# Optimization experiments

Hardware: AMD Instinct MI355X
Metric: run time of the kernel (lower is better)

## Reference

```python
import math
import jax, jax.numpy as jnp
import numpy as np

C = 1024
H = 8
EPS = 1e-5
SLOPE = 0.1


def _branch(x, W, gamma, beta, mean, var):
    # conv1x1 (no bias) -> BatchNorm1d (eval-mode stats) -> LeakyReLU(0.1)
    # x: [b, C, p], W: [C_out, C_in]
    y = jnp.einsum('oc,bcp->bop', W, x)
    scale = gamma / jnp.sqrt(var + EPS)          # [C]
    y = y * scale[:, None] + (beta - mean * scale)[:, None]
    return jnp.where(y > 0, y, SLOPE * y)


def setup_inputs() -> dict:
    key = jax.random.key(0)
    ks = jax.random.split(key, 20)
    b, pq, pk = 4, 2048, 2048
    d = {
        'Xq': jax.random.normal(ks[0], (b, C, pq), dtype=jnp.float32),
        'Xk': jax.random.normal(ks[1], (b, C, pk), dtype=jnp.float32),
        'Wq': jax.random.normal(ks[2], (C, C), dtype=jnp.float32) * (1.0 / math.sqrt(C)),
        'Wk': jax.random.normal(ks[3], (C, C), dtype=jnp.float32) * (1.0 / math.sqrt(C)),
        'Wv': jax.random.normal(ks[4], (C, C), dtype=jnp.float32) * (1.0 / math.sqrt(C)),
    }
    for i, tag in enumerate(['1', '2', '3']):
        d['gamma' + tag] = jnp.ones((C,), jnp.float32) + 0.1 * jax.random.normal(ks[5 + 4 * i], (C,), jnp.float32)
        d['beta' + tag] = 0.1 * jax.random.normal(ks[6 + 4 * i], (C,), jnp.float32)
        d['mean' + tag] = 0.1 * jax.random.normal(ks[7 + 4 * i], (C,), jnp.float32)
        d['var' + tag] = 0.5 + jax.random.uniform(ks[8 + 4 * i], (C,), jnp.float32)
    return d


def reference(Xq, Xk, Wq, Wk, Wv,
              gamma1, beta1, mean1, var1,
              gamma2, beta2, mean2, var2,
              gamma3, beta3, mean3, var3):
    Q = _branch(Xq, Wq, gamma1, beta1, mean1, var1)   # [b, C, pq]
    K = _branch(Xk, Wk, gamma2, beta2, mean2, var2)   # [b, C, pk]
    V = _branch(Xq, Wv, gamma3, beta3, mean3, var3)   # [b, C, pq]
    b, c, pk = K.shape
    pq = V.shape[-1]
    dh = c // H
    Qh = Q.reshape(b, H, dh, pq)
    Kh = K.reshape(b, H, dh, pk)
    Vh = V.reshape(b, H, dh, pq)
    # scores over channel dim: [b, h, pk, pq]
    Hmat = jnp.einsum('bhci,bhcj->bhij', Kh, Vh) / math.sqrt(c / H)
    Hmat = jax.nn.softmax(Hmat, axis=-1)
    out = jnp.einsum('bhij,bhcj->bhci', Hmat, Qh)     # [b, h, dh, pk]
    return out.reshape(b, c, pk)
```

## Files before the change

kernel.cpp:

```cpp
#include <hip/hip_runtime.h>

typedef __bf16 bf16_t;
typedef __bf16 bf16x8 __attribute__((ext_vector_type(8)));
typedef __bf16 bf16x4 __attribute__((ext_vector_type(4)));
typedef float  f32x4  __attribute__((ext_vector_type(4)));

#define WB_OFF  0LL
#define XQT_OFF 3145728LL
#define XKT_OFF 11534336LL
#define Q_OFF   19922944LL
#define KT_OFF  28311552LL
#define VT_OFF  36700160LL

__device__ __forceinline__ void gl_lds16(const bf16_t* g, bf16_t* l) {
  __builtin_amdgcn_global_load_lds((const __attribute__((address_space(1))) void*)(g),
                                   (__attribute__((address_space(3))) void*)(l), 16, 0, 0);
}

__device__ __forceinline__ bf16x4 cvt4(f32x4 v) {
  bf16x4 r;
  r[0] = (bf16_t)v[0]; r[1] = (bf16_t)v[1]; r[2] = (bf16_t)v[2]; r[3] = (bf16_t)v[3];
  return r;
}

__global__ __launch_bounds__(256) void k_wconv(
    const float* __restrict__ Wq, const float* __restrict__ Wk, const float* __restrict__ Wv,
    bf16_t* __restrict__ ws)
{
  const float* W = blockIdx.y == 0 ? Wq : (blockIdx.y == 1 ? Wk : Wv);
  bf16_t* dst = ws + WB_OFF + (long)blockIdx.y * 1048576;
  const long i = ((long)blockIdx.x * 256 + threadIdx.x) * 4;
  *(bf16x4*)&dst[i] = cvt4(*(const f32x4*)(W + i));
}

__global__ __launch_bounds__(256) void k_transpose(
    const float* __restrict__ Xq, const float* __restrict__ Xk, bf16_t* __restrict__ ws)
{
  __shared__ __align__(16) bf16_t t[64 * 72];
  const int z = blockIdx.z, b = z & 3, ts = z >> 2;
  const float* X = ts ? Xk : Xq;
  bf16_t* XT = ws + (ts ? XKT_OFF : XQT_OFF);
  const int p0 = blockIdx.x * 64, c0 = blockIdx.y * 64;
  const int tid = threadIdx.x;
  const int tx = tid & 15, ty = tid >> 4;
  const float* src = X + ((long)b * 1024 + c0) * 2048 + p0;
  #pragma unroll
  for (int hh = 0; hh < 4; ++hh) {
    int c = ty + hh * 16;
    f32x4 v = *(const f32x4*)(src + (long)c * 2048 + tx * 4);
    *(bf16x4*)&t[c * 72 + tx * 4] = cvt4(v);
  }
  __syncthreads();
  bf16_t* dst = XT + ((long)b * 2048 + p0) * 1024 + c0;
  #pragma unroll
  for (int hh = 0; hh < 2; ++hh) {
    int p = (tid >> 3) + hh * 32;
    int cc = tid & 7;
    bf16x8 v;
    #pragma unroll
    for (int j = 0; j < 8; ++j) v[j] = t[(cc * 8 + j) * 72 + p];
    *(bf16x8*)(dst + (long)p * 1024 + cc * 8) = v;
  }
}

__global__ __launch_bounds__(256) void k_qkv(
    const float* __restrict__ g1, const float* __restrict__ b1, const float* __restrict__ m1, const float* __restrict__ v1,
    const float* __restrict__ g2, const float* __restrict__ b2, const float* __restrict__ m2, const float* __restrict__ v2,
    const float* __restrict__ g3, const float* __restrict__ b3, const float* __restrict__ m3, const float* __restrict__ v3,
    bf16_t* __restrict__ ws)
{
  __shared__ __align__(16) bf16_t smem[17408];
  bf16_t* sa = smem;
  bf16_t* sb = smem + 8192;
  bf16_t* ep = smem;
  __shared__ float sS[128], sBi[128];

  const int tid = threadIdx.x;
  const int z = blockIdx.z, br = z >> 2, b = z & 3;
  const int o0 = blockIdx.y * 128, p0 = blockIdx.x * 128;

  const float *gm, *bt, *mn, *vr;
  const bf16_t *XT;
  bf16_t* dst;
  int tr;
  if (br == 0)      { XT = ws + XQT_OFF; gm = g1; bt = b1; mn = m1; vr = v1; dst = ws + Q_OFF;  tr = 0; }
  else if (br == 1) { XT = ws + XKT_OFF; gm = g2; bt = b2; mn = m2; vr = v2; dst = ws + KT_OFF; tr = 1; }
  else              { XT = ws + XQT_OFF; gm = g3; bt = b3; mn = m3; vr = v3; dst = ws + VT_OFF; tr = 1; }
  const bf16_t* W = ws + WB_OFF + (long)br * 1048576;

  if (tid < 128) {
    float g = gm[o0 + tid], be = bt[o0 + tid];
    float m = mn[o0 + tid], v = vr[o0 + tid];
    float sc = g / sqrtf(v + 1e-5f);
    sS[tid] = sc; sBi[tid] = be - m * sc;
  }

  const int w = tid >> 6, lane = tid & 63, quad = lane >> 4, l15 = lane & 15;
  const int wr = (w >> 1) * 64, wc = (w & 1) * 64;

  f32x4 acc[4][4];
  #pragma unroll
  for (int i = 0; i < 4; ++i)
    #pragma unroll
    for (int j = 0; j < 4; ++j) acc[i][j] = f32x4{0.f, 0.f, 0.f, 0.f};

  const bf16_t* Wb = W + (long)o0 * 1024;
  const bf16_t* Xb = XT + ((long)b * 2048 + p0) * 1024;

  for (int kk = 0; kk < 16; ++kk) {
    __syncthreads();
    const int kof = kk * 64;
    #pragma unroll
    for (int is = 0; is < 4; ++is) {
      int s = (is * 4 + w) * 64 + lane;
      int row = s >> 3, ch = s & 7;
      int col = kof + ((ch ^ (row & 7)) << 3);
      gl_lds16(Wb + (long)row * 1024 + col, &sa[(is * 4 + w) * 512]);
      gl_lds16(Xb + (long)row * 1024 + col, &sb[(is * 4 + w) * 512]);
    }
    __syncthreads();
    #pragma unroll
    for (int ks = 0; ks < 2; ++ks) {
      bf16x8 af[4], bfr[4];
      #pragma unroll
      for (int i = 0; i < 4; ++i) {
        int mm = wr + i * 16 + l15;
        af[i] = *(const bf16x8*)&sa[mm * 64 + (((ks * 4 + quad) ^ (mm & 7)) << 3)];
        int nn = wc + i * 16 + l15;
        bfr[i] = *(const bf16x8*)&sb[nn * 64 + (((ks * 4 + quad) ^ (nn & 7)) << 3)];
      }
      #pragma unroll
      for (int i = 0; i < 4; ++i)
        #pragma unroll
        for (int j = 0; j < 4; ++j)
          acc[i][j] = __builtin_amdgcn_mfma_f32_16x16x32_bf16(af[i], bfr[j], acc[i][j], 0, 0, 0);
    }
  }

  __syncthreads();
  #pragma unroll
  for (int i = 0; i < 4; ++i) {
    #pragma unroll
    for (int j = 0; j < 4; ++j) {
      const int p_l = wc + j * 16 + l15;
      const int ob = wr + i * 16 + quad * 4;
      if (!tr) {
        #pragma unroll
        for (int r = 0; r < 4; ++r) {
          float v = fmaf(acc[i][j][r], sS[ob + r], sBi[ob + r]);
          v = v > 0.f ? v : 0.1f * v;
          ep[(ob + r) * 136 + p_l] = (bf16_t)v;
        }
      } else {
        bf16x4 t4;
        #pragma unroll
        for (int r = 0; r < 4; ++r) {
          float v = fmaf(acc[i][j][r], sS[ob + r], sBi[ob + r]);
          v = v > 0.f ? v : 0.1f * v;
          t4[r] = (bf16_t)v;
        }
        *(bf16x4*)&ep[p_l * 136 + ob] = t4;
      }
    }
  }
  __syncthreads();
  #pragma unroll
  for (int pass = 0; pass < 8; ++pass) {
    int row = pass * 16 + (tid >> 4);
    int ch = tid & 15;
    bf16x8 v = *(const bf16x8*)&ep[row * 136 + ch * 8];
    long off;
    if (!tr) off = ((long)b * 1024 + o0 + row) * 2048 + p0 + ch * 8;
    else     off = ((long)b * 2048 + p0 + row) * 1024 + o0 + ch * 8;
    *(bf16x8*)&dst[off] = v;
  }
}

__global__ __launch_bounds__(512, 4) void k_attn(const bf16_t* __restrict__ ws, float* __restrict__ out)
{
  __shared__ __align__(16) bf16_t sV[2][8192];
  __shared__ __align__(16) bf16_t sQ[2][8192];
  __shared__ __align__(16) bf16_t sP[8192];

  const int tid = threadIdx.x, w = tid >> 6, lane = tid & 63, quad = lane >> 4, l15 = lane & 15;
  const int i0 = blockIdx.x * 128, h = blockIdx.y, b = blockIdx.z;

  const bf16_t* KTb = ws + KT_OFF + ((long)b * 2048 + i0) * 1024 + h * 128;
  const bf16_t* VTb = ws + VT_OFF + ((long)b * 2048) * 1024 + h * 128;
  const bf16_t* Qb  = ws + Q_OFF  + ((long)b * 1024 + h * 128) * 2048;

  const int irow = w * 16 + l15;

  bf16x8 af[4];
  #pragma unroll
  for (int ks = 0; ks < 4; ++ks)
    af[ks] = *(const bf16x8*)(KTb + (long)irow * 1024 + (ks * 4 + quad) * 8);

  f32x4 U[8];
  #pragma unroll
  for (int f = 0; f < 8; ++f) U[f] = f32x4{0.f, 0.f, 0.f, 0.f};
  float ls = 0.f;

  const float SCL = 1.4426950408889634f * 0.08838834764831843f;

  #define STAGE(jt, bb)                                                               \
    {                                                                                 \
      const int j0_ = (jt) * 64;                                                      \
      _Pragma("unroll")                                                               \
      for (int rnd = 0; rnd < 2; ++rnd) {                                             \
        int s = rnd * 512 + tid;                                                      \
        int vrow = s >> 4, vch = s & 15;                                              \
        gl_lds16(VTb + (long)(j0_ + vrow) * 1024 + ((vch ^ (vrow & 15)) << 3),        \
                 &sV[bb][s * 8]);                                                     \
        int qrow = s >> 3, qch = s & 7;                                               \
        gl_lds16(Qb + (long)qrow * 2048 + j0_ + ((qch ^ (qrow & 7)) << 3),            \
                 &sQ[bb][s * 8]);                                                     \
      }                                                                               \
    }

  STAGE(0, 0);
  __syncthreads();

  for (int jt = 0; jt < 32; ++jt) {
    const int cur = jt & 1;
    if (jt < 31) STAGE(jt + 1, cur ^ 1);

    #pragma unroll
    for (int fj = 0; fj < 4; ++fj) {
      f32x4 S = f32x4{0.f, 0.f, 0.f, 0.f};
      const int jr = fj * 16 + l15;
      #pragma unroll
      for (int ks = 0; ks < 4; ++ks) {
        bf16x8 vfr = *(const bf16x8*)&sV[cur][jr * 128 + (((ks * 4 + quad) ^ (jr & 15)) << 3)];
        S = __builtin_amdgcn_mfma_f32_16x16x32_bf16(vfr, af[ks], S, 0, 0, 0);
      }
      bf16x4 p4;
      #pragma unroll
      for (int r = 0; r < 4; ++r) {
        float p = exp2f(S[r] * SCL);
        ls += p;
        p4[r] = (bf16_t)p;
      }
      const int i = w * 16 + l15;
      const int jl = fj * 16 + quad * 4;
      *(bf16x4*)&sP[i * 64 + (((jl >> 3) ^ (i & 7)) << 3) + (jl & 7)] = p4;
    }

    bf16x8 pf[2];
    #pragma unroll
    for (int ks = 0; ks < 2; ++ks)
      pf[ks] = *(const bf16x8*)&sP[irow * 64 + (((ks * 4 + quad) ^ (irow & 7)) << 3)];

    #pragma unroll
    for (int fc = 0; fc < 8; ++fc) {
      const int c = fc * 16 + l15;
      #pragma unroll
      for (int ks = 0; ks < 2; ++ks) {
        bf16x8 qf = *(const bf16x8*)&sQ[cur][c * 64 + (((ks * 4 + quad) ^ (c & 7)) << 3)];
        U[fc] = __builtin_amdgcn_mfma_f32_16x16x32_bf16(pf[ks], qf, U[fc], 0, 0, 0);
      }
    }
    __syncthreads();
  }

  ls += __shfl_xor(ls, 16, 64);
  ls += __shfl_xor(ls, 32, 64);
  float* lsum = (float*)&sP[(w * 16) * 64];
  if (quad == 0) lsum[l15] = ls;
  f32x4 rl4 = *(const f32x4*)&lsum[quad * 4];

  #pragma unroll
  for (int fc = 0; fc < 8; ++fc) {
    const int c = h * 128 + fc * 16 + l15;
    f32x4 v;
    #pragma unroll
    for (int r = 0; r < 4; ++r) v[r] = U[fc][r] / rl4[r];
    const long o = ((long)b * 1024 + c) * 2048 + i0 + w * 16 + quad * 4;
    *(f32x4*)&out[o] = v;
  }
}

extern "C" void kernel_launch(void* const* d_in, const int* in_sizes, int n_in,
                              void* d_out, int out_size, void* d_ws, size_t ws_size,
                              hipStream_t stream)
{
  (void)in_sizes; (void)n_in; (void)out_size; (void)ws_size;
  const float* Xq = (const float*)d_in[0];
  const float* Xk = (const float*)d_in[1];
  const float* Wq = (const float*)d_in[2];
  const float* Wk = (const float*)d_in[3];
  const float* Wv = (const float*)d_in[4];
  bf16_t* ws = (bf16_t*)d_ws;
  float* out = (float*)d_out;

  k_wconv<<<dim3(1024, 3), 256, 0, stream>>>(Wq, Wk, Wv, ws);
  k_transpose<<<dim3(32, 16, 8), 256, 0, stream>>>(Xq, Xk, ws);
  k_qkv<<<dim3(16, 8, 12), 256, 0, stream>>>(
      (const float*)d_in[5],  (const float*)d_in[6],  (const float*)d_in[7],  (const float*)d_in[8],
      (const float*)d_in[9],  (const float*)d_in[10], (const float*)d_in[11], (const float*)d_in[12],
      (const float*)d_in[13], (const float*)d_in[14], (const float*)d_in[15], (const float*)d_in[16],
      ws);
  k_attn<<<dim3(16, 8, 4), 512, 0, stream>>>(ws, out);
}
```

Before: 292.1 us.

## Retile attention block into 2x4 warp grid with 32x32 subtiles for fragment reuse

The 8 warps are reorganized from 16-row strips into a 4x2 grid. Each warp computes a 32x32 score subtile and a 32x64 output subtile, so V/K and P/Q fragments loaded from LDS are reused across two MFMAs instead of one. This adds an extra barrier per iteration, because P rows are now produced by different warps. Row sums are combined across the two j-groups through shared memory. Global load addresses are precomputed and advanced incrementally, and the final divide is replaced by a reciprocal multiply.

Measured after the change: 299.0 us. 1.02x slower.

```diff
diff --git a/kernel.cpp b/kernel.cpp
--- a/kernel.cpp
+++ b/kernel.cpp
@@ -189,94 +189,127 @@
   const bf16_t* VTb = ws + VT_OFF + ((long)b * 2048) * 1024 + h * 128;
   const bf16_t* Qb  = ws + Q_OFF  + ((long)b * 1024 + h * 128) * 2048;
 
-  const int irow = w * 16 + l15;
-
-  bf16x8 af[4];
-  #pragma unroll
-  for (int ks = 0; ks < 4; ++ks)
-    af[ks] = *(const bf16x8*)(KTb + (long)irow * 1024 + (ks * 4 + quad) * 8);
-
-  f32x4 U[8];
-  #pragma unroll
-  for (int f = 0; f < 8; ++f) U[f] = f32x4{0.f, 0.f, 0.f, 0.f};
-  float ls = 0.f;
+  const int iq = w & 3, jg = w >> 2;
+  const int i0w = iq * 32, j0w = jg * 32, c0 = jg * 64;
+
+  bf16x8 kf[2][4];
+  #pragma unroll
+  for (int ng = 0; ng < 2; ++ng) {
+    const bf16_t* kr = KTb + (long)(i0w + ng * 16 + l15) * 1024 + quad * 8;
+    #pragma unroll
+    for (int kc = 0; kc < 4; ++kc)
+      kf[ng][kc] = *(const bf16x8*)(kr + kc * 32);
+  }
+
+  f32x4 U[2][4];
+  #pragma unroll
+  for (int ig = 0; ig < 2; ++ig)
+    #pragma unroll
+    for (int ng = 0; ng < 4; ++ng) U[ig][ng] = f32x4{0.f, 0.f, 0.f, 0.f};
+  float ls2[2] = {0.f, 0.f};
+
+  const int sA = tid, sB = 512 + tid;
+  const bf16_t* vgA = VTb + (long)(sA >> 4) * 1024 + (((sA & 15) ^ ((sA >> 4) & 15)) << 3);
+  const bf16_t* vgB = VTb + (long)(sB >> 4) * 1024 + (((sB & 15) ^ ((sB >> 4) & 15)) << 3);
+  const bf16_t* qgA = Qb + (long)(sA >> 3) * 2048 + (((sA & 7) ^ ((sA >> 3) & 7)) << 3);
+  const bf16_t* qgB = Qb + (long)(sB >> 3) * 2048 + (((sB & 7) ^ ((sB >> 3) & 7)) << 3);
+
+  auto stage = [&](int bb) {
+    gl_lds16(vgA, &sV[bb][sA * 8]);
+    gl_lds16(qgA, &sQ[bb][sA * 8]);
+    gl_lds16(vgB, &sV[bb][sB * 8]);
+    gl_lds16(qgB, &sQ[bb][sB * 8]);
+    vgA += 65536; vgB += 65536;
+    qgA += 64;    qgB += 64;
+  };
 
   const float SCL = 1.4426950408889634f * 0.08838834764831843f;
 
-  #define STAGE(jt, bb)                                                               \
-    {                                                                                 \
-      const int j0_ = (jt) * 64;                                                      \
-      _Pragma("unroll")                                                               \
-      for (int rnd = 0; rnd < 2; ++rnd) {                                             \
-        int s = rnd * 512 + tid;                                                      \
-        int vrow = s >> 4, vch = s & 15;                                              \
-        gl_lds16(VTb + (long)(j0_ + vrow) * 1024 + ((vch ^ (vrow & 15)) << 3),        \
-                 &sV[bb][s * 8]);                                                     \
-        int qrow = s >> 3, qch = s & 7;                                               \
-        gl_lds16(Qb + (long)qrow * 2048 + j0_ + ((qch ^ (qrow & 7)) << 3),            \
-                 &sQ[bb][s * 8]);                                                     \
-      }                                                                               \
-    }
-
-  STAGE(0, 0);
+  stage(0);
   __syncthreads();
 
   for (int jt = 0; jt < 32; ++jt) {
     const int cur = jt & 1;
-    if (jt < 31) STAGE(jt + 1, cur ^ 1);
-
-    #pragma unroll
-    for (int fj = 0; fj < 4; ++fj) {
-      f32x4 S = f32x4{0.f, 0.f, 0.f, 0.f};
-      const int jr = fj * 16 + l15;
-      #pragma unroll
-      for (int ks = 0; ks < 4; ++ks) {
-        bf16x8 vfr = *(const bf16x8*)&sV[cur][jr * 128 + (((ks * 4 + quad) ^ (jr & 15)) << 3)];
-        S = __builtin_amdgcn_mfma_f32_16x16x32_bf16(vfr, af[ks], S, 0, 0, 0);
-      }
-      bf16x4 p4;
-      #pragma unroll
-      for (int r = 0; r < 4; ++r) {
-        float p = exp2f(S[r] * SCL);
-        ls += p;
-        p4[r] = (bf16_t)p;
-      }
-      const int i = w * 16 + l15;
-      const int jl = fj * 16 + quad * 4;
-      *(bf16x4*)&sP[i * 64 + (((jl >> 3) ^ (i & 7)) << 3) + (jl & 7)] = p4;
-    }
-
-    bf16x8 pf[2];
-    #pragma unroll
-    for (int ks = 0; ks < 2; ++ks)
-      pf[ks] = *(const bf16x8*)&sP[irow * 64 + (((ks * 4 + quad) ^ (irow & 7)) << 3)];
-
-    #pragma unroll
-    for (int fc = 0; fc < 8; ++fc) {
-      const int c = fc * 16 + l15;
-      #pragma unroll
-      for (int ks = 0; ks < 2; ++ks) {
-        bf16x8 qf = *(const bf16x8*)&sQ[cur][c * 64 + (((ks * 4 + quad) ^ (c & 7)) << 3)];
-        U[fc] = __builtin_amdgcn_mfma_f32_16x16x32_bf16(pf[ks], qf, U[fc], 0, 0, 0);
+    if (jt < 31) stage(cur ^ 1);
+
+    const bf16_t* sVc = sV[cur];
+    #pragma unroll
+    for (int mg = 0; mg < 2; ++mg) {
+      const int j = j0w + mg * 16 + l15;
+      bf16x8 av[4];
+      #pragma unroll
+      for (int kc = 0; kc < 4; ++kc)
+        av[kc] = *(const bf16x8*)&sVc[j * 128 + (((kc * 4 + quad) ^ l15) << 3)];
+      #pragma unroll
+      for (int ng = 0; ng < 2; ++ng) {
+        f32x4 S = f32x4{0.f, 0.f, 0.f, 0.f};
+        #pragma unroll
+        for (int kc = 0; kc < 4; ++kc)
+          S = __builtin_amdgcn_mfma_f32_16x16x32_bf16(av[kc], kf[ng][kc], S, 0, 0, 0);
+        bf16x4 p4;
+        #pragma unroll
+        for (int r = 0; r < 4; ++r) {
+          float p = exp2f(S[r] * SCL);
+          ls2[ng] += p;
+          p4[r] = (bf16_t)p;
+        }
+        const int i = i0w + ng * 16 + l15;
+        const int jw = j0w + mg * 16 + quad * 4;
+        *(bf16x4*)&sP[i * 64 + (((jw >> 3) ^ (i & 7)) << 3) + (jw & 7)] = p4;
       }
     }
     __syncthreads();
-  }
-
-  ls += __shfl_xor(ls, 16, 64);
-  ls += __shfl_xor(ls, 32, 64);
-  float* lsum = (float*)&sP[(w * 16) * 64];
-  if (quad == 0) lsum[l15] = ls;
-  f32x4 rl4 = *(const f32x4*)&lsum[quad * 4];
-
-  #pragma unroll
-  for (int fc = 0; fc < 8; ++fc) {
-    const int c = h * 128 + fc * 16 + l15;
-    f32x4 v;
-    #pragma unroll
-    for (int r = 0; r < 4; ++r) v[r] = U[fc][r] / rl4[r];
-    const long o = ((long)b * 1024 + c) * 2048 + i0 + w * 16 + quad * 4;
-    *(f32x4*)&out[o] = v;
+
+    const bf16_t* sQc = sQ[cur];
+    #pragma unroll
+    for (int kj = 0; kj < 2; ++kj) {
+      bf16x8 pa[2];
+      #pragma unroll
+      for (int ig = 0; ig < 2; ++ig) {
+        const int i = i0w + ig * 16 + l15;
+        pa[ig] = *(const bf16x8*)&sP[i * 64 + (((kj * 4 + quad) ^ (i & 7)) << 3)];
+      }
+      #pragma unroll
+      for (int ng = 0; ng < 4; ++ng) {
+        const int c = c0 + ng * 16 + l15;
+        bf16x8 qf = *(const bf16x8*)&sQc[c * 64 + (((kj * 4 + quad) ^ (c & 7)) << 3)];
+        #pragma unroll
+        for (int ig = 0; ig < 2; ++ig)
+          U[ig][ng] = __builtin_amdgcn_mfma_f32_16x16x32_bf16(pa[ig], qf, U[ig][ng], 0, 0, 0);
+      }
+    }
+    __syncthreads();
+  }
+
+  #pragma unroll
+  for (int ng = 0; ng < 2; ++ng) {
+    ls2[ng] += __shfl_xor(ls2[ng], 16, 64);
+    ls2[ng] += __shfl_xor(ls2[ng], 32, 64);
+  }
+  float* lsb = (float*)sP;
+  if (lane < 16) {
+    lsb[jg * 128 + i0w + lane] = ls2[0];
+    lsb[jg * 128 + i0w + 16 + lane] = ls2[1];
+  }
+  __syncthreads();
+
+  #pragma unroll
+  for (int ig = 0; ig < 2; ++ig) {
+    f32x4 rcp;
+    #pragma unroll
+    for (int r = 0; r < 4; ++r) {
+      const int i = i0w + ig * 16 + quad * 4 + r;
+      rcp[r] = 1.0f / (lsb[i] + lsb[128 + i]);
+    }
+    #pragma unroll
+    for (int ng = 0; ng < 4; ++ng) {
+      const int c = h * 128 + c0 + ng * 16 + l15;
+      f32x4 v;
+      #pragma unroll
+      for (int r = 0; r < 4; ++r) v[r] = U[ig][ng][r] * rcp[r];
+      const long o = ((long)b * 1024 + c) * 2048 + i0 + i0w + ig * 16 + quad * 4;
+      *(f32x4*)&out[o] = v;
+    }
   }
 }
 
```
